# Kernel tuning notes

Hardware: AMD Instinct MI355X
Metric: run time of the kernel (lower is better)

Reference implementation:

```python
import jax, jax.numpy as jnp
import numpy as np

DIM_IN = 32
DIM_OUT = 32
DIM_X = 64   # dim_internal
DIM_NL = 32
EPS_Q = 1e-4      # eps in default Q
TOL = 1e-3        # pos_def_tol
D22_EPS = 1.0     # d22_epsilon


def _model_param(X, Y, B2, C2, D12, D22_L, D22_U, D21, gamma):
    """Faithful port of REN_IQC_gamma._update_model_param (QR_fun=None, dim_in==dim_out)."""
    g = gamma[0, 0]
    Q = -EPS_Q * jnp.eye(DIM_OUT)
    R = -2.0 * g * jnp.eye(DIM_IN)
    S = jnp.eye(DIM_OUT, DIM_IN)
    # D22 = base + sym + skew (dim_in == dim_out)
    D22 = (g + D22_EPS) * jnp.eye(DIM_OUT, DIM_IN) + D22_L.T @ D22_L + (D22_U - D22_U.T)
    SD = S @ D22
    R_cal = R + SD + SD.T + D22.T @ Q @ D22
    R_cal_inv = jnp.linalg.inv(R_cal)
    M = D22.T @ Q + S
    C2_cal = M @ C2                      # (dim_in, dim_x)
    D21_cal = M @ D21 - D12.T            # (dim_in, dim_nl)
    vec_r = jnp.concatenate([C2_cal.T, D21_cal.T, B2], axis=0)   # (2*dim_x+dim_nl, dim_in)
    psi_r = vec_r @ R_cal_inv @ vec_r.T
    vec_q = jnp.concatenate([C2.T, D21.T, jnp.zeros((DIM_X, DIM_OUT), X.dtype)], axis=0)
    psi_q = vec_q @ Q @ vec_q.T
    n = 2 * DIM_X + DIM_NL
    H = X.T @ X + TOL * jnp.eye(n) + psi_r - psi_q
    i1, i2 = DIM_X, DIM_X + DIM_NL
    H11 = H[:i1, :i1]
    H21 = H[i1:i2, :i1]
    H22 = H[i1:i2, i1:i2]
    H31 = H[i2:, :i1]
    H32 = H[i2:, i1:i2]
    H33 = H[i2:, i2:]
    E = 0.5 * (H11 + H33 + Y - Y.T)
    E_inv = jnp.linalg.inv(E)
    Lam = 0.5 * jnp.diag(H22)            # Lambda (dim_nl,)
    D11 = -jnp.tril(H22, k=-1)           # strictly lower triangular
    C1 = -H21
    Fm = H31
    B1 = H32
    return Fm, B1, E_inv, Lam, D11, C1, D22


def reference(u_in, x0, X, Y, B2, C2, D12, D22_L, D22_U, D21, gamma):
    # Parameters are constant across time steps, so the per-step recompute in the
    # torch code collapses to a single evaluation with identical math.
    Fm, B1, E_inv, Lam, D11, C1, D22 = _model_param(X, Y, B2, C2, D12, D22_L, D22_U, D21, gamma)
    B = u_in.shape[0]
    nl_idx = jnp.arange(DIM_NL)

    def step(x, u_t):                    # x: (B, DIM_X), u_t: (B, DIM_IN)
        a = x @ C1.T + u_t @ D12.T       # (B, DIM_NL), constant part of v

        def inner(w, i):                 # forward substitution over strictly-lower D11
            v = a[:, i] + w @ D11[i]     # (B,)
            w = w.at[:, i].set(jnp.tanh(v / Lam[i]))
            return w, None

        w, _ = jax.lax.scan(inner, jnp.zeros((B, DIM_NL), u_in.dtype), nl_idx)
        x_new = (x @ Fm.T + w @ B1.T + u_t @ B2.T) @ E_inv.T
        y_t = x_new @ C2.T + w @ D21.T + u_t @ D22.T
        return x_new, y_t

    u_time = jnp.swapaxes(u_in, 0, 1)    # (T, B, DIM_IN)
    _, ys = jax.lax.scan(step, x0[:, 0, :], u_time)
    return jnp.swapaxes(ys, 0, 1)        # (B, T, DIM_OUT)


def setup_inputs() -> dict:
    key = jax.random.key(0)
    ks = jax.random.split(key, 10)
    std = 0.5
    n = 2 * DIM_X + DIM_NL
    B, T = 2048, 256
    return {
        "u_in": jax.random.normal(ks[0], (B, T, DIM_IN), jnp.float32),
        "x0": jax.random.normal(ks[1], (B, 1, DIM_X), jnp.float32),
        "X": jax.random.normal(ks[2], (n, n), jnp.float32) * std,
        "Y": jax.random.normal(ks[3], (DIM_X, DIM_X), jnp.float32) * std,
        "B2": jax.random.normal(ks[4], (DIM_X, DIM_IN), jnp.float32) * std,
        "C2": jax.random.normal(ks[5], (DIM_OUT, DIM_X), jnp.float32) * std,
        "D12": jax.random.normal(ks[6], (DIM_NL, DIM_IN), jnp.float32) * std,
        "D22_L": jax.random.normal(ks[7], (DIM_IN, DIM_IN), jnp.float32) * std,
        "D22_U": jax.random.normal(ks[8], (DIM_OUT, DIM_IN), jnp.float32) * std,
        "D21": jnp.zeros((DIM_OUT, DIM_NL), jnp.float32),   # registered buffer, fixed zero
        "gamma": jax.random.normal(ks[9], (1, 1), jnp.float32) * 3.0,
    }
```

## Files before the change

kernel.cpp:

```cpp
#include <hip/hip_runtime.h>
#include <math.h>

#define EPS_Q 1e-4
#define TOLC  1e-3

#define OFF_D22   0
#define OFF_RINV  1024
#define OFF_VR    2048
#define OFF_T1    7168
#define OFF_H     12288
#define OFF_E     37888
#define OFF_EI    41984
#define OFF_TMP   46080
#define OFF_TMP2  50176
#define D_END     54272

__global__ __launch_bounds__(256, 1) void prep1(
    const float* __restrict__ B2, const float* __restrict__ C2,
    const float* __restrict__ D12, const float* __restrict__ L,
    const float* __restrict__ U, const float* __restrict__ D21,
    const float* __restrict__ gam, double* __restrict__ wsd)
{
  __shared__ double aug[32][65];
  __shared__ double sFac[32];
  __shared__ int sPiv;
  const int tid = threadIdx.x;
  const double g = (double)gam[0];
  double* D22d = wsd + OFF_D22;

  for (int idx = tid; idx < 1024; idx += 256) {
    int i = idx >> 5, j = idx & 31;
    double s = (i == j) ? (g + 1.0) : 0.0;
    for (int k = 0; k < 32; ++k) s += (double)L[k*32+i] * (double)L[k*32+j];
    s += (double)U[i*32+j] - (double)U[j*32+i];
    D22d[idx] = s;
  }
  __syncthreads();
  for (int idx = tid; idx < 1024; idx += 256) {
    int i = idx >> 5, j = idx & 31;
    double s = (i == j) ? (-2.0 * g) : 0.0;
    s += D22d[i*32+j] + D22d[j*32+i];
    double q = 0.0;
    for (int k = 0; k < 32; ++k) q += D22d[k*32+i] * D22d[k*32+j];
    aug[i][j] = s - EPS_Q * q;
    aug[i][32+j] = (i == j) ? 1.0 : 0.0;
  }
  __syncthreads();
  for (int k = 0; k < 32; ++k) {
    if (tid < 64) {
      float mv = -1.f; int mi = k;
      if (tid < 32 && tid >= k) { mv = (float)fabs(aug[tid][k]); mi = tid; }
      #pragma unroll
      for (int o = 32; o; o >>= 1) {
        float ov = __shfl_xor(mv, o); int oi = __shfl_xor(mi, o);
        if (ov > mv) { mv = ov; mi = oi; }
      }
      if (tid == 0) sPiv = mi;
    }
    __syncthreads();
    int p = sPiv;
    if (p != k) for (int c = tid; c < 64; c += 256) { double t1 = aug[k][c]; aug[k][c] = aug[p][c]; aug[p][c] = t1; }
    __syncthreads();
    double pinv = 1.0 / aug[k][k];
    if (tid < 32 && tid != k) sFac[tid] = aug[tid][k];
    __syncthreads();
    for (int c = tid; c < 64; c += 256) aug[k][c] *= pinv;
    __syncthreads();
    for (int idx = tid; idx < 2048; idx += 256) {
      int r = idx >> 6, c = idx & 63;
      if (r != k) aug[r][c] -= sFac[r] * aug[k][c];
    }
    __syncthreads();
  }
  double* Rinv = wsd + OFF_RINV;
  for (int idx = tid; idx < 1024; idx += 256) Rinv[idx] = aug[idx >> 5][32 + (idx & 31)];

  double* vr = wsd + OFF_VR;
  for (int idx = tid; idx < 64*32; idx += 256) {
    int p = idx >> 5, k = idx & 31;
    double q = 0.0;
    for (int m = 0; m < 32; ++m) q += D22d[m*32+k] * (double)C2[m*64+p];
    vr[p*32+k] = (double)C2[k*64+p] - EPS_Q * q;
  }
  for (int idx = tid; idx < 32*32; idx += 256) {
    int p = idx >> 5, k = idx & 31;
    double q = 0.0;
    for (int m = 0; m < 32; ++m) q += D22d[m*32+k] * (double)D21[m*32+p];
    vr[(64+p)*32+k] = (double)D21[k*32+p] - EPS_Q * q - (double)D12[p*32+k];
  }
  for (int idx = tid; idx < 64*32; idx += 256) {
    int p = idx >> 5, k = idx & 31;
    vr[(96+p)*32+k] = (double)B2[p*32+k];
  }
  __syncthreads();
  double* T1 = wsd + OFF_T1;
  for (int idx = tid; idx < 160*32; idx += 256) {
    int p = idx >> 5, k2 = idx & 31;
    double s = 0.0;
    for (int k = 0; k < 32; ++k) s += vr[p*32+k] * Rinv[k*32+k2];
    T1[idx] = s;
  }
}

__global__ __launch_bounds__(256, 1) void prep2(
    const float* __restrict__ X, const float* __restrict__ C2,
    const float* __restrict__ D21, double* __restrict__ wsd)
{
  const double* vr = wsd + OFF_VR;
  const double* T1 = wsd + OFF_T1;
  double* H = wsd + OFF_H;
  int bi = blockIdx.x / 10, bj = blockIdx.x % 10;
  int i = bi*16 + (threadIdx.x >> 4);
  int j = bj*16 + (threadIdx.x & 15);
  double s = (i == j) ? TOLC : 0.0;
  for (int k = 0; k < 160; ++k) s += (double)X[k*160+i] * (double)X[k*160+j];
  double pr = 0.0;
  for (int k = 0; k < 32; ++k) pr += T1[i*32+k] * vr[j*32+k];
  s += pr;
  if (i < 96 && j < 96) {
    double vq = 0.0;
    for (int k = 0; k < 32; ++k) {
      double a = (i < 64) ? (double)C2[k*64+i] : (double)D21[k*32+(i-64)];
      double b = (j < 64) ? (double)C2[k*64+j] : (double)D21[k*32+(j-64)];
      vq += a*b;
    }
    s += EPS_Q * vq;
  }
  H[i*160+j] = s;
}

__global__ __launch_bounds__(1024, 1) void prep3(
    const float* __restrict__ Y, const float* __restrict__ B2,
    const float* __restrict__ C2, const float* __restrict__ D12,
    const float* __restrict__ D21, double* __restrict__ wsd)
{
  __shared__ float aug[64][130];
  __shared__ float sFac[64];
  __shared__ int sPiv;
  const int tid = threadIdx.x;
  double* H   = wsd + OFF_H;
  double* Ed  = wsd + OFF_E;
  double* Ei  = wsd + OFF_EI;
  double* Tm  = wsd + OFF_TMP;
  double* Tm2 = wsd + OFF_TMP2;
  double* D22d = wsd + OFF_D22;
  float* fb = (float*)(wsd + D_END);
  const double KS = 2.8853900817779268;

  for (int idx = tid; idx < 4096; idx += 1024) {
    int i = idx >> 6, j = idx & 63;
    double e = 0.5*(H[i*160+j] + H[(96+i)*160+(96+j)] + (double)Y[i*64+j] - (double)Y[j*64+i]);
    Ed[idx] = e;
    aug[i][j] = (float)e;
    aug[i][64+j] = (i == j) ? 1.f : 0.f;
  }
  __syncthreads();
  for (int k = 0; k < 64; ++k) {
    if (tid < 64) {
      float mv = -1.f; int mi = k;
      if (tid >= k) { mv = fabsf(aug[tid][k]); mi = tid; }
      #pragma unroll
      for (int o = 32; o; o >>= 1) {
        float ov = __shfl_xor(mv, o); int oi = __shfl_xor(mi, o);
        if (ov > mv) { mv = ov; mi = oi; }
      }
      if (tid == 0) sPiv = mi;
    }
    __syncthreads();
    int p = sPiv;
    if (p != k) for (int c = tid; c < 128; c += 1024) { float t1 = aug[k][c]; aug[k][c] = aug[p][c]; aug[p][c] = t1; }
    __syncthreads();
    float pinv = 1.0f / aug[k][k];
    if (tid < 64 && tid != k) sFac[tid] = aug[tid][k];
    __syncthreads();
    for (int c = tid; c < 128; c += 1024) aug[k][c] *= pinv;
    __syncthreads();
    for (int idx = tid; idx < 64*128; idx += 1024) {
      int r = idx >> 7, c = idx & 127;
      if (r != k) aug[r][c] -= sFac[r] * aug[k][c];
    }
    __syncthreads();
  }
  for (int idx = tid; idx < 4096; idx += 1024) Ei[idx] = (double)aug[idx >> 6][64 + (idx & 63)];
  __syncthreads();
  for (int it = 0; it < 2; ++it) {
    for (int idx = tid; idx < 4096; idx += 1024) {
      int i = idx >> 6, j = idx & 63;
      double s = (i == j) ? 2.0 : 0.0;
      for (int k = 0; k < 64; ++k) s -= Ed[i*64+k] * Ei[k*64+j];
      Tm[idx] = s;
    }
    __syncthreads();
    for (int idx = tid; idx < 4096; idx += 1024) {
      int i = idx >> 6, j = idx & 63;
      double s = 0.0;
      for (int k = 0; k < 64; ++k) s += Ei[i*64+k] * Tm[k*64+j];
      Tm2[idx] = s;
    }
    __syncthreads();
    for (int idx = tid; idx < 4096; idx += 1024) Ei[idx] = Tm2[idx];
    __syncthreads();
  }
  for (int idx = tid; idx < 64*128; idx += 1024) {
    int r = idx >> 7, col = idx & 127;
    double s = 0.0;
    if (col < 64)       { for (int k = 0; k < 64; ++k) s += Ei[r*64+k] * H[(96+k)*160 + col]; }
    else if (col < 96)  { int jj = col-64; for (int k = 0; k < 64; ++k) s += Ei[r*64+k] * H[(96+k)*160 + 64 + jj]; }
    else                { int jj = col-96; for (int k = 0; k < 64; ++k) s += Ei[r*64+k] * (double)B2[k*32+jj]; }
    fb[((col >> 2)*64 + r)*4 + (col & 3)] = (float)s;
  }
  for (int idx = tid; idx < 32*128; idx += 1024) {
    int r = idx >> 7, col = idx & 127;
    float v;
    if (col < 64)      v = C2[r*64 + col];
    else if (col < 96) v = D21[r*32 + (col-64)];
    else               v = (float)D22d[r*32 + (col-96)];
    fb[8192 + ((col >> 2)*32 + r)*4 + (col & 3)] = v;
  }
  for (int idx = tid; idx < 1024; idx += 1024) {
    int i = idx >> 5, j = idx & 31;
    double li = 2.0 / H[(64+i)*160 + 64+i];
    fb[12288 + idx] = (j < i) ? (float)(-H[(64+i)*160 + 64+j] * li * KS) : 0.f;
  }
  for (int idx = tid; idx < 32*96; idx += 1024) {
    int r = idx / 96, j = idx % 96;
    double li = 2.0 / H[(64+r)*160 + 64+r];
    double v = (j < 64) ? (-H[(64+r)*160 + j] * li) : ((double)D12[r*32 + (j-64)] * li);
    fb[13312 + idx] = (float)(v * KS);
  }
}

__device__ __forceinline__ float frcp(float x) {
#if __has_builtin(__builtin_amdgcn_rcpf)
  return __builtin_amdgcn_rcpf(x);
#else
  return 1.0f / x;
#endif
}
__device__ __forceinline__ float hsum4(float4 a) { return (a.x + a.y) + (a.z + a.w); }

#define PIN(x) asm volatile("" : "+v"(x))
__global__ __launch_bounds__(256, 1) void ren_main(
    const float* __restrict__ u_in, const float* __restrict__ x0,
    const double* __restrict__ wsd, float* __restrict__ out)
{
  __shared__ __align__(16) float sW[8192];
  __shared__ __align__(16) float sXU[4][132];
  const float* fb = (const float*)(wsd + D_END);
  const int tid = threadIdx.x;
  {
    const float4* g4 = (const float4*)fb;
    float4* s4 = (float4*)sW;
    for (int i = tid; i < 1024; i += 256) s4[i] = g4[2048 + i];
    for (int i = tid; i < 768; i += 256) {
      int r2 = i / 24, ch = i % 24;
      s4[1024 + ch*32 + r2] = g4[3328 + i];
    }
    if (tid < 256) s4[1792 + tid] = g4[1792 + tid];
  }
  const int wv = tid >> 6, l = tid & 63;
  const int r = l & 31, lh = l >> 5;
  const int e = blockIdx.x * 4 + wv;
  float* xu = &sXU[wv][0];

  float4 wx[28];
  {
    const float4* WxG = (const float4*)fb;
    #pragma unroll
    for (int c = 0; c < 28; ++c) wx[c] = WxG[(c << 6) + l];
  }
  float d11[32];
  {
    const float4* DG = (const float4*)(fb + 12288);
    #pragma unroll
    for (int c = 0; c < 8; ++c) {
      float4 dv = DG[r*8 + c];
      d11[4*c+0] = dv.x; d11[4*c+1] = dv.y; d11[4*c+2] = dv.z; d11[4*c+3] = dv.w;
    }
  }
  #pragma unroll
  for (int c = 0; c < 28; ++c) {
    PIN(wx[c].x); PIN(wx[c].y); PIN(wx[c].z); PIN(wx[c].w);
  }
  #pragma unroll
  for (int j = 0; j < 32; ++j) PIN(d11[j]);

  xu[l] = x0[(size_t)e*64 + l];
  xu[96 + r] = u_in[(size_t)e*8192 + r];
  __syncthreads();

  const float4* xu4  = (const float4*)xu;
  const float4* WyT4 = (const float4*)sW;
  const float4* WaT4 = (const float4*)sW + 1024;
  const float4* sWx4 = (const float4*)sW + 1792;
  const float* uG = u_in + (size_t)e * 8192;
  float* oG = out + (size_t)e * 8192;

#define FMA4(A, W, XV) \
  A.x = fmaf(W.x, XV.x, A.x); A.y = fmaf(W.y, XV.y, A.y); \
  A.z = fmaf(W.z, XV.z, A.z); A.w = fmaf(W.w, XV.w, A.w);

  for (int t = 0; t < 256; ++t) {
    const int tn = (t < 255) ? (t + 1) : 255;
    float unext = uG[tn*32 + r];
    float4 sA = make_float4(0.f, 0.f, 0.f, 0.f);
    #pragma unroll
    for (int c = 0; c < 12; ++c) {
      int ch = lh*12 + c;
      int xi = (ch < 16) ? ch : (ch + 8);
      float4 xv = xu4[xi]; float4 wv4 = WaT4[ch*32 + r];
      FMA4(sA, wv4, xv)
    }
    float a = hsum4(sA);
    a += __shfl_xor(a, 32);
    float4 P4 = make_float4(0.f, 0.f, 0.f, 0.f);
    #pragma unroll
    for (int c = 0; c < 16; ++c) { float4 xv = xu4[c]; FMA4(P4, wx[c], xv) }
    #pragma unroll
    for (int c = 24; c < 28; ++c) { float4 xv = xu4[c]; FMA4(P4, wx[c], xv) }
    #pragma unroll
    for (int c = 28; c < 32; ++c) { float4 xv = xu4[c]; float4 wv4 = sWx4[((c - 28) << 6) + l]; FMA4(P4, wv4, xv) }
    float4 Q4 = make_float4(0.f, 0.f, 0.f, 0.f);
    #pragma unroll
    for (int c = 0; c < 4; ++c) {
      int ch = 24 + lh*4 + c;
      float4 xv = xu4[ch]; float4 wv4 = WyT4[(ch << 5) + r];
      FMA4(Q4, wv4, xv)
    }
    float v = a;
    #pragma unroll
    for (int j = 0; j < 31; ++j) {
      float E = __builtin_exp2f(v);
      float w = fmaf(-2.f, frcp(E + 1.f), 1.f);
      float b = __int_as_float(__builtin_amdgcn_readlane(__float_as_int(w), j));
      v = fmaf(d11[j], b, v);
    }
    float Ef = __builtin_exp2f(v);
    float myw = fmaf(-2.f, frcp(Ef + 1.f), 1.f);
    xu[64 + r] = myw;
    #pragma unroll
    for (int c = 16; c < 24; ++c) { float4 xv = xu4[c]; FMA4(P4, wx[c], xv) }
    xu[l] = hsum4(P4);
    #pragma unroll
    for (int c = 0; c < 12; ++c) {
      int ch = lh*12 + c;
      float4 xv = xu4[ch]; float4 wv4 = WyT4[(ch << 5) + r];
      FMA4(Q4, wv4, xv)
    }
    float y = hsum4(Q4);
    y += __shfl_xor(y, 32);
    if (l < 32) oG[t*32 + l] = y;
    xu[96 + r] = unext;
  }
#undef FMA4
}
#undef PIN

extern "C" void kernel_launch(void* const* d_in, const int* in_sizes, int n_in,
                              void* d_out, int out_size, void* d_ws, size_t ws_size,
                              hipStream_t stream)
{
  const float* u_in = (const float*)d_in[0];
  const float* x0   = (const float*)d_in[1];
  const float* X    = (const float*)d_in[2];
  const float* Y    = (const float*)d_in[3];
  const float* B2   = (const float*)d_in[4];
  const float* C2   = (const float*)d_in[5];
  const float* D12  = (const float*)d_in[6];
  const float* L    = (const float*)d_in[7];
  const float* U    = (const float*)d_in[8];
  const float* D21  = (const float*)d_in[9];
  const float* gam  = (const float*)d_in[10];
  double* wsd = (double*)d_ws;
  float* out = (float*)d_out;

  hipLaunchKernelGGL(prep1, dim3(1), dim3(256), 0, stream, B2, C2, D12, L, U, D21, gam, wsd);
  hipLaunchKernelGGL(prep2, dim3(100), dim3(256), 0, stream, X, C2, D21, wsd);
  hipLaunchKernelGGL(prep3, dim3(1), dim3(1024), 0, stream, Y, B2, C2, D12, D21, wsd);
  hipLaunchKernelGGL(ren_main, dim3(512), dim3(256), 0, stream, u_in, x0, wsd, out);
}
```

Before: 1.366 ms.

## Fuse parameter prep kernels into one block and split out XᵀX

The three serial prep kernels are merged into two. A multi-block XᵀX kernel writes the base of H. A single 1024-thread block then does the R inverse, the vec_r products, the psi corrections to H, and the E inversion and refinement. This removes one kernel launch and raises the thread count of the former 256-thread prep stage. In exchange, the 160x160 psi_r/psi_q update now runs inside one workgroup instead of across 100 blocks. The prep stage is probably small next to the main recurrent kernel, so little change is expected.

```diff
diff --git a/kernel.cpp b/kernel.cpp
--- a/kernel.cpp
+++ b/kernel.cpp
@@ -15,20 +15,35 @@
 #define OFF_TMP2  50176
 #define D_END     54272
 
-__global__ __launch_bounds__(256, 1) void prep1(
+__global__ __launch_bounds__(256, 1) void xtx(
+    const float* __restrict__ X, double* __restrict__ wsd)
+{
+  double* H = wsd + OFF_H;
+  int bi = blockIdx.x / 10, bj = blockIdx.x % 10;
+  int i = bi*16 + (threadIdx.x >> 4);
+  int j = bj*16 + (threadIdx.x & 15);
+  double s = (i == j) ? TOLC : 0.0;
+  for (int k = 0; k < 160; ++k) s += (double)X[k*160+i] * (double)X[k*160+j];
+  H[i*160+j] = s;
+}
+
+__global__ __launch_bounds__(1024, 1) void prep_fused(
     const float* __restrict__ B2, const float* __restrict__ C2,
     const float* __restrict__ D12, const float* __restrict__ L,
     const float* __restrict__ U, const float* __restrict__ D21,
-    const float* __restrict__ gam, double* __restrict__ wsd)
+    const float* __restrict__ gam, const float* __restrict__ Y,
+    double* __restrict__ wsd)
 {
-  __shared__ double aug[32][65];
-  __shared__ double sFac[32];
+  __shared__ double aug1[32][65];
+  __shared__ float  aug[64][130];
+  __shared__ double sFacD[32];
+  __shared__ float  sFacF[64];
   __shared__ int sPiv;
   const int tid = threadIdx.x;
   const double g = (double)gam[0];
   double* D22d = wsd + OFF_D22;
 
-  for (int idx = tid; idx < 1024; idx += 256) {
+  for (int idx = tid; idx < 1024; idx += 1024) {
     int i = idx >> 5, j = idx & 31;
     double s = (i == j) ? (g + 1.0) : 0.0;
     for (int k = 0; k < 32; ++k) s += (double)L[k*32+i] * (double)L[k*32+j];
@@ -36,20 +51,20 @@
     D22d[idx] = s;
   }
   __syncthreads();
-  for (int idx = tid; idx < 1024; idx += 256) {
+  for (int idx = tid; idx < 1024; idx += 1024) {
     int i = idx >> 5, j = idx & 31;
     double s = (i == j) ? (-2.0 * g) : 0.0;
     s += D22d[i*32+j] + D22d[j*32+i];
     double q = 0.0;
     for (int k = 0; k < 32; ++k) q += D22d[k*32+i] * D22d[k*32+j];
-    aug[i][j] = s - EPS_Q * q;
-    aug[i][32+j] = (i == j) ? 1.0 : 0.0;
+    aug1[i][j] = s - EPS_Q * q;
+    aug1[i][32+j] = (i == j) ? 1.0 : 0.0;
   }
   __syncthreads();
   for (int k = 0; k < 32; ++k) {
     if (tid < 64) {
       float mv = -1.f; int mi = k;
-      if (tid < 32 && tid >= k) { mv = (float)fabs(aug[tid][k]); mi = tid; }
+      if (tid < 32 && tid >= k) { mv = (float)fabs(aug1[tid][k]); mi = tid; }
       #pragma unroll
       for (int o = 32; o; o >>= 1) {
         float ov = __shfl_xor(mv, o); int oi = __shfl_xor(mi, o);
@@ -59,91 +74,72 @@
     }
     __syncthreads();
     int p = sPiv;
-    if (p != k) for (int c = tid; c < 64; c += 256) { double t1 = aug[k][c]; aug[k][c] = aug[p][c]; aug[p][c] = t1; }
-    __syncthreads();
-    double pinv = 1.0 / aug[k][k];
-    if (tid < 32 && tid != k) sFac[tid] = aug[tid][k];
-    __syncthreads();
-    for (int c = tid; c < 64; c += 256) aug[k][c] *= pinv;
-    __syncthreads();
-    for (int idx = tid; idx < 2048; idx += 256) {
+    if (p != k) for (int c = tid; c < 64; c += 1024) { double t1 = aug1[k][c]; aug1[k][c] = aug1[p][c]; aug1[p][c] = t1; }
+    __syncthreads();
+    double pinv = 1.0 / aug1[k][k];
+    if (tid < 32 && tid != k) sFacD[tid] = aug1[tid][k];
+    __syncthreads();
+    for (int c = tid; c < 64; c += 1024) aug1[k][c] *= pinv;
+    __syncthreads();
+    for (int idx = tid; idx < 2048; idx += 1024) {
       int r = idx >> 6, c = idx & 63;
-      if (r != k) aug[r][c] -= sFac[r] * aug[k][c];
+      if (r != k) aug1[r][c] -= sFacD[r] * aug1[k][c];
     }
     __syncthreads();
   }
   double* Rinv = wsd + OFF_RINV;
-  for (int idx = tid; idx < 1024; idx += 256) Rinv[idx] = aug[idx >> 5][32 + (idx & 31)];
+  for (int idx = tid; idx < 1024; idx += 1024) Rinv[idx] = aug1[idx >> 5][32 + (idx & 31)];
 
   double* vr = wsd + OFF_VR;
-  for (int idx = tid; idx < 64*32; idx += 256) {
+  for (int idx = tid; idx < 64*32; idx += 1024) {
     int p = idx >> 5, k = idx & 31;
     double q = 0.0;
     for (int m = 0; m < 32; ++m) q += D22d[m*32+k] * (double)C2[m*64+p];
     vr[p*32+k] = (double)C2[k*64+p] - EPS_Q * q;
   }
-  for (int idx = tid; idx < 32*32; idx += 256) {
+  for (int idx = tid; idx < 32*32; idx += 1024) {
     int p = idx >> 5, k = idx & 31;
     double q = 0.0;
     for (int m = 0; m < 32; ++m) q += D22d[m*32+k] * (double)D21[m*32+p];
     vr[(64+p)*32+k] = (double)D21[k*32+p] - EPS_Q * q - (double)D12[p*32+k];
   }
-  for (int idx = tid; idx < 64*32; idx += 256) {
+  for (int idx = tid; idx < 64*32; idx += 1024) {
     int p = idx >> 5, k = idx & 31;
     vr[(96+p)*32+k] = (double)B2[p*32+k];
   }
   __syncthreads();
   double* T1 = wsd + OFF_T1;
-  for (int idx = tid; idx < 160*32; idx += 256) {
+  for (int idx = tid; idx < 160*32; idx += 1024) {
     int p = idx >> 5, k2 = idx & 31;
     double s = 0.0;
     for (int k = 0; k < 32; ++k) s += vr[p*32+k] * Rinv[k*32+k2];
     T1[idx] = s;
   }
-}
-
-__global__ __launch_bounds__(256, 1) void prep2(
-    const float* __restrict__ X, const float* __restrict__ C2,
-    const float* __restrict__ D21, double* __restrict__ wsd)
-{
-  const double* vr = wsd + OFF_VR;
-  const double* T1 = wsd + OFF_T1;
-  double* H = wsd + OFF_H;
-  int bi = blockIdx.x / 10, bj = blockIdx.x % 10;
-  int i = bi*16 + (threadIdx.x >> 4);
-  int j = bj*16 + (threadIdx.x & 15);
-  double s = (i == j) ? TOLC : 0.0;
-  for (int k = 0; k < 160; ++k) s += (double)X[k*160+i] * (double)X[k*160+j];
-  double pr = 0.0;
-  for (int k = 0; k < 32; ++k) pr += T1[i*32+k] * vr[j*32+k];
-  s += pr;
-  if (i < 96 && j < 96) {
-    double vq = 0.0;
-    for (int k = 0; k < 32; ++k) {
-      double a = (i < 64) ? (double)C2[k*64+i] : (double)D21[k*32+(i-64)];
-      double b = (j < 64) ? (double)C2[k*64+j] : (double)D21[k*32+(j-64)];
-      vq += a*b;
-    }
-    s += EPS_Q * vq;
-  }
-  H[i*160+j] = s;
-}
-
-__global__ __launch_bounds__(1024, 1) void prep3(
-    const float* __restrict__ Y, const float* __restrict__ B2,
-    const float* __restrict__ C2, const float* __restrict__ D12,
-    const float* __restrict__ D21, double* __restrict__ wsd)
-{
-  __shared__ float aug[64][130];
-  __shared__ float sFac[64];
-  __shared__ int sPiv;
-  const int tid = threadIdx.x;
+  __syncthreads();
+  for (int idx = tid; idx < 25600; idx += 1024) {
+    int i = idx / 160, j = idx % 160;
+    double* H = wsd + OFF_H;
+    double pr = 0.0;
+    for (int k = 0; k < 32; ++k) pr += T1[i*32+k] * vr[j*32+k];
+    double s = H[i*160+j] + pr;
+    if (i < 96 && j < 96) {
+      double vq = 0.0;
+      for (int k = 0; k < 32; ++k) {
+        double a = (i < 64) ? (double)C2[k*64+i] : (double)D21[k*32+(i-64)];
+        double b = (j < 64) ? (double)C2[k*64+j] : (double)D21[k*32+(j-64)];
+        vq += a*b;
+      }
+      s += EPS_Q * vq;
+    }
+    H[i*160+j] = s;
+  }
+  __syncthreads();
+
   double* H   = wsd + OFF_H;
   double* Ed  = wsd + OFF_E;
   double* Ei  = wsd + OFF_EI;
   double* Tm  = wsd + OFF_TMP;
   double* Tm2 = wsd + OFF_TMP2;
-  double* D22d = wsd + OFF_D22;
   float* fb = (float*)(wsd + D_END);
   const double KS = 2.8853900817779268;
 
@@ -171,13 +167,13 @@
     if (p != k) for (int c = tid; c < 128; c += 1024) { float t1 = aug[k][c]; aug[k][c] = aug[p][c]; aug[p][c] = t1; }
     __syncthreads();
     float pinv = 1.0f / aug[k][k];
-    if (tid < 64 && tid != k) sFac[tid] = aug[tid][k];
+    if (tid < 64 && tid != k) sFacF[tid] = aug[tid][k];
     __syncthreads();
     for (int c = tid; c < 128; c += 1024) aug[k][c] *= pinv;
     __syncthreads();
     for (int idx = tid; idx < 64*128; idx += 1024) {
       int r = idx >> 7, c = idx & 127;
-      if (r != k) aug[r][c] -= sFac[r] * aug[k][c];
+      if (r != k) aug[r][c] -= sFacF[r] * aug[k][c];
     }
     __syncthreads();
   }
@@ -374,8 +370,8 @@
   double* wsd = (double*)d_ws;
   float* out = (float*)d_out;
 
-  hipLaunchKernelGGL(prep1, dim3(1), dim3(256), 0, stream, B2, C2, D12, L, U, D21, gam, wsd);
-  hipLaunchKernelGGL(prep2, dim3(100), dim3(256), 0, stream, X, C2, D21, wsd);
-  hipLaunchKernelGGL(prep3, dim3(1), dim3(1024), 0, stream, Y, B2, C2, D12, D21, wsd);
+  hipLaunchKernelGGL(xtx, dim3(100), dim3(256), 0, stream, X, wsd);
+  hipLaunchKernelGGL(prep_fused, dim3(1), dim3(1024), 0, stream,
+                     B2, C2, D12, L, U, D21, gam, Y, wsd);
   hipLaunchKernelGGL(ren_main, dim3(512), dim3(256), 0, stream, u_in, x0, wsd, out);
 }
```

Result: slower. 1.587 ms (+16.2%).
